# Kernel tuning notes

Measured on AMD Instinct MI355X. Metric: run time of the kernel, lower is better.

The kernel has to match this reference:

```python
import jax, jax.numpy as jnp
import numpy as np
from jax import lax

D_MODEL = 1024
D_STATE = 16
D_CONV = 4
D_INNER = 2 * D_MODEL
BATCH = 2
SEQ = 1024


def setup_inputs() -> dict:
    key = jax.random.key(0)
    ks = jax.random.split(key, 8)
    std = 0.02
    return {
        "x": jax.random.normal(ks[0], (BATCH, SEQ, D_MODEL), jnp.float32),
        "in_proj_w": jax.random.normal(ks[1], (2 * D_INNER, D_MODEL), jnp.float32) * std,
        "conv_w": jax.random.normal(ks[2], (D_INNER, 1, D_CONV), jnp.float32) * 0.1,
        "x_proj_w": jax.random.normal(ks[3], (D_STATE + 1, D_INNER), jnp.float32) * std,
        "dt_w": jax.random.normal(ks[4], (D_INNER, 1), jnp.float32) * std,
        "dt_b": jnp.zeros((D_INNER,), jnp.float32),
        "A_param": jax.random.normal(ks[5], (D_INNER, D_STATE), jnp.float32) * std,
        "D_param": jnp.ones((D_INNER,), jnp.float32),
        "out_w": jax.random.normal(ks[6], (D_MODEL, D_INNER), jnp.float32) * std,
        "out_b": jnp.zeros((D_MODEL,), jnp.float32),
    }


def _silu(v):
    return v * jax.nn.sigmoid(v)


def _mamba_forward(x, in_proj_w, conv_w, x_proj_w, dt_w, dt_b, A_param, D_param, out_w, out_b):
    B, L, _ = x.shape
    # in_proj: [B,L,2*d_inner]
    xz = jnp.einsum('bld,ed->ble', x, in_proj_w)
    u, z = jnp.split(xz, 2, axis=-1)  # each [B,L,d_inner]
    # depthwise causal conv1d along time
    uc = u.transpose(0, 2, 1)  # [B,d_inner,L]
    uc = lax.conv_general_dilated(
        uc, conv_w, window_strides=(1,), padding=[(D_CONV - 1, D_CONV - 1)],
        dimension_numbers=('NCH', 'OIH', 'NCH'), feature_group_count=D_INNER,
    )[:, :, :L]
    u = _silu(uc.transpose(0, 2, 1))  # [B,L,d_inner]
    # x_proj -> (dt scalar, B coeffs)
    x_dbl = jnp.einsum('bld,ed->ble', u, x_proj_w)  # [B,L,d_state+1]
    dt_in = x_dbl[..., :1]                          # [B,L,1]
    Bmat = x_dbl[..., 1:]                           # [B,L,d_state]
    delta = jax.nn.softplus(dt_in * dt_w[:, 0] + dt_b)  # [B,L,d_inner]
    A = -jnp.exp(A_param)                            # [d_inner,d_state]

    # selective scan (time-major lax.scan)
    def step(h, inp):
        d_t, b_t = inp  # [B,d_inner], [B,d_state]
        h = jnp.exp(A * d_t[..., None]) * h + d_t[..., None] * b_t[:, None, :]
        y = jnp.einsum('bdn,bn->bd', h, b_t)
        return h, y

    h0 = jnp.zeros((B, D_INNER, D_STATE), x.dtype)
    _, ys = lax.scan(step, h0, (delta.transpose(1, 0, 2), Bmat.transpose(1, 0, 2)))
    y = ys.transpose(1, 0, 2) + u * D_param  # [B,L,d_inner]
    y = y * _silu(z)
    return jnp.einsum('bld,ed->ble', y, out_w) + out_b


def reference(x, in_proj_w, conv_w, x_proj_w, dt_w, dt_b, A_param, D_param, out_w, out_b):
    return _mamba_forward(x, in_proj_w, conv_w, x_proj_w, dt_w, dt_b, A_param, D_param, out_w, out_b)
```

## Files before the change

kernel.cpp:

```cpp
#include <hip/hip_runtime.h>
#include <stdint.h>
#include <stddef.h>

#define D_MODEL 1024
#define D_STATE 16
#define D_INNER 2048
#define BATCH   2
#define SEQ     1024
#define MROWS   (BATCH*SEQ)

#define NCH 16
#define TCH (SEQ/NCH)
#define NREC (BATCH*D_INNER*D_STATE)

typedef __bf16 bf16x8 __attribute__((ext_vector_type(8)));
typedef float  f32x4  __attribute__((ext_vector_type(4)));
typedef unsigned short u16x8 __attribute__((ext_vector_type(8)));

__device__ __forceinline__ unsigned short f2bf(float f) {
    unsigned int u = __float_as_uint(f);
    u += 0x7fffu + ((u >> 16) & 1u);
    return (unsigned short)(u >> 16);
}
__device__ __forceinline__ float bf2f(unsigned short v) {
    return __uint_as_float((unsigned int)v << 16);
}

__device__ __forceinline__ void gl_lds16(const unsigned short* g, unsigned short* l) {
    __builtin_amdgcn_global_load_lds(
        (const __attribute__((address_space(1))) unsigned int*)g,
        (__attribute__((address_space(3))) unsigned int*)l, 16, 0, 0);
}

__global__ void cvt_all_kernel(const float* __restrict__ x,
                               const float* __restrict__ w1,
                               const float* __restrict__ w2,
                               const float* __restrict__ xw,
                               unsigned short* __restrict__ xb,
                               unsigned short* __restrict__ wbi,
                               unsigned short* __restrict__ wbo,
                               unsigned short* __restrict__ wbp) {
    int blk = blockIdx.x, tid = threadIdx.x;
    if (blk < 8192) {
        const float* src; unsigned short* dst; int i;
        if (blk < 2048)      { src = x;  dst = xb;  i = blk * 1024 + tid * 4; }
        else if (blk < 6144) { src = w1; dst = wbi; i = (blk - 2048) * 1024 + tid * 4; }
        else                 { src = w2; dst = wbo; i = (blk - 6144) * 1024 + tid * 4; }
        float4 v = *(const float4*)(src + i);
        ushort4 o;
        o.x = f2bf(v.x); o.y = f2bf(v.y); o.z = f2bf(v.z); o.w = f2bf(v.w);
        *(ushort4*)(dst + i) = o;
    } else {
        int id = (blk - 8192) * 256 + tid;
        wbp[id] = (id < 17 * D_INNER) ? f2bf(xw[id]) : (unsigned short)0;
    }
}

template<int NT, bool SPLITK2, bool OUT_BF16>
__global__ void gemm_bf16_kernel(const unsigned short* __restrict__ A,
                                 const unsigned short* __restrict__ Bw,
                                 void* __restrict__ Cv,
                                 int M, int N, int K) {
    constexpr int NTW = NT / 32;
    constexpr int BCH = NT / 8;
    __shared__ __align__(16) unsigned short Al[2][2 * 128 * 32];
    __shared__ __align__(16) unsigned short Bl[2][2 * NT * 32];

    const int tid  = threadIdx.x;
    const int lane = tid & 63;
    const int wid  = tid >> 6;
    const int wm   = wid >> 1;
    const int wn   = wid & 1;
    const int ln   = lane & 15;
    const int q    = lane >> 4;
    const int mblk = blockIdx.y * 128;
    const int nblk = blockIdx.x * NT;
    const int srow = lane >> 2;
    const int spart = lane & 3;

    const int kbeg = SPLITK2 ? blockIdx.z * (K / 2) : 0;
    const int kend = SPLITK2 ? kbeg + K / 2 : K;

    f32x4 acc[4][NTW] = {};

    auto stage = [&](int buf, int k0) {
        #pragma unroll
        for (int h = 0; h < 4; ++h) {
            int j = wid * 4 + h;
            int kh = j & 1, rb = j >> 1;
            int row = rb * 16 + srow;
            gl_lds16(A + (size_t)(mblk + row) * K + k0 + kh * 32 + spart * 8,
                     Al[buf] + kh * 4096 + rb * 512);
        }
        #pragma unroll
        for (int h = 0; h < BCH / 4; ++h) {
            int j = wid * (BCH / 4) + h;
            int kh = j & 1, rb = j >> 1;
            int row = rb * 16 + srow;
            gl_lds16(Bw + (size_t)(nblk + row) * K + k0 + kh * 32 + spart * 8,
                     Bl[buf] + kh * (NT * 32) + rb * 512);
        }
    };

    stage(0, kbeg);
    __syncthreads();
    int cur = 0;

    for (int k0 = kbeg; k0 < kend; k0 += 64) {
        if (k0 + 64 < kend) stage(cur ^ 1, k0 + 64);

        #pragma unroll
        for (int kh = 0; kh < 2; ++kh) {
            bf16x8 af[4], bfr[NTW];
            #pragma unroll
            for (int mt = 0; mt < 4; ++mt)
                af[mt] = *(const bf16x8*)(Al[cur] + kh * 4096 + (wm * 64 + mt * 16 + ln) * 32 + q * 8);
            #pragma unroll
            for (int nt = 0; nt < NTW; ++nt)
                bfr[nt] = *(const bf16x8*)(Bl[cur] + kh * (NT * 32) + (wn * (NT/2) + nt * 16 + ln) * 32 + q * 8);
            #pragma unroll
            for (int mt = 0; mt < 4; ++mt)
                #pragma unroll
                for (int nt = 0; nt < NTW; ++nt)
                    acc[mt][nt] = __builtin_amdgcn_mfma_f32_16x16x32_bf16(
                        af[mt], bfr[nt], acc[mt][nt], 0, 0, 0);
        }
        __syncthreads();
        cur ^= 1;
    }

    size_t cofs = SPLITK2 ? (size_t)blockIdx.z * M * N : 0;
    #pragma unroll
    for (int mt = 0; mt < 4; ++mt) {
        #pragma unroll
        for (int nt = 0; nt < NTW; ++nt) {
            int col = nblk + wn * (NT/2) + nt * 16 + ln;
            #pragma unroll
            for (int r = 0; r < 4; ++r) {
                int row = mblk + wm * 64 + mt * 16 + q * 4 + r;
                if (OUT_BF16)
                    ((unsigned short*)Cv)[cofs + (size_t)row * N + col] = f2bf(acc[mt][nt][r]);
                else
                    ((float*)Cv)[cofs + (size_t)row * N + col] = acc[mt][nt][r];
            }
        }
    }
}

__global__ void splitk_reduce_kernel(const float* __restrict__ part,
                                     const float* __restrict__ bias,
                                     float* __restrict__ out) {
    int i = (blockIdx.x * 256 + threadIdx.x) * 4;
    int n = i & (D_MODEL - 1);
    float4 a = *(const float4*)(part + i);
    float4 b = *(const float4*)(part + (size_t)MROWS * D_MODEL + i);
    float4 bv = *(const float4*)(bias + n);
    float4 o;
    o.x = a.x + b.x + bv.x; o.y = a.y + b.y + bv.y;
    o.z = a.z + b.z + bv.z; o.w = a.w + b.w + bv.w;
    *(float4*)(out + i) = o;
}

__global__ void conv_xproj_kernel(const unsigned short* __restrict__ xzb,
                                  const float* __restrict__ conv_w,
                                  const unsigned short* __restrict__ wbp,
                                  unsigned short* __restrict__ ub,
                                  float* __restrict__ dti,
                                  float* __restrict__ Bm) {
    __shared__ float red[4][17];
    const int tid = threadIdx.x;
    const int m = blockIdx.x;
    const int l = m & (SEQ - 1);
    const int d = tid * 8;
    const int lane = tid & 63;
    const int wid  = tid >> 6;

    const float4* wv = (const float4*)(conv_w + (size_t)d * 4);
    float4 w[8];
    #pragma unroll
    for (int e = 0; e < 8; ++e) w[e] = wv[e];
    float s[8] = {0.f, 0.f, 0.f, 0.f, 0.f, 0.f, 0.f, 0.f};
    #pragma unroll
    for (int j = 0; j < 4; ++j) {
        if (l - j >= 0) {
            u16x8 r = *(const u16x8*)(xzb + (size_t)(m - j) * 4096 + d);
            #pragma unroll
            for (int e = 0; e < 8; ++e) {
                float wt = (j == 0) ? w[e].w : (j == 1) ? w[e].z
                         : (j == 2) ? w[e].y : w[e].x;
                s[e] += wt * bf2f(r[e]);
            }
        }
    }
    float u[8];
    u16x8 o;
    #pragma unroll
    for (int e = 0; e < 8; ++e) {
        float sig = 1.f / (1.f + __expf(-s[e]));
        u[e] = s[e] * sig;
        o[e] = f2bf(u[e]);
    }
    *(u16x8*)(ub + (size_t)m * D_INNER + d) = o;

    #pragma unroll
    for (int n = 0; n < 17; ++n) {
        u16x8 wn = *(const u16x8*)(wbp + (size_t)n * D_INNER + d);
        float p = 0.f;
        #pragma unroll
        for (int e = 0; e < 8; ++e) p += u[e] * bf2f(wn[e]);
        #pragma unroll
        for (int off = 32; off > 0; off >>= 1)
            p += __shfl_xor(p, off, 64);
        if (lane == 0) red[wid][n] = p;
    }
    __syncthreads();
    if (tid < 17) {
        float ssum = red[0][tid] + red[1][tid] + red[2][tid] + red[3][tid];
        if (tid == 0) dti[m] = ssum;
        else Bm[(size_t)m * D_STATE + (tid - 1)] = ssum;
    }
}

__device__ __forceinline__ float softplus_f(float xv) {
    return fmaxf(xv, 0.f) + __logf(1.f + __expf(-fabsf(xv)));
}

__global__ void scanA_kernel(const float* __restrict__ dt_in,
                             const float* __restrict__ Bm,
                             const float* __restrict__ dt_w,
                             const float* __restrict__ dt_b,
                             const float* __restrict__ A_param,
                             float* __restrict__ Pg,
                             float* __restrict__ Sg) {
    __shared__ float sdt[TCH];
    __shared__ float sB[TCH * D_STATE];
    const int tid = threadIdx.x;
    const int b = blockIdx.z, c = blockIdx.y;
    const int d = blockIdx.x * 256 + tid;

    if (tid < TCH) sdt[tid] = dt_in[b * SEQ + c * TCH + tid];
    ((float4*)sB)[tid] = ((const float4*)(Bm + ((size_t)(b * SEQ + c * TCH)) * D_STATE))[tid];
    __syncthreads();

    const float dtw = dt_w[d], dtb = dt_b[d];
    float aA[D_STATE], h[D_STATE];
    #pragma unroll
    for (int n4 = 0; n4 < 4; ++n4) {
        float4 ap = ((const float4*)(A_param + (size_t)d * D_STATE))[n4];
        aA[n4*4+0] = -__expf(ap.x); aA[n4*4+1] = -__expf(ap.y);
        aA[n4*4+2] = -__expf(ap.z); aA[n4*4+3] = -__expf(ap.w);
    }
    #pragma unroll
    for (int n = 0; n < D_STATE; ++n) h[n] = 0.f;
    float tsum = 0.f;

    for (int t = 0; t < TCH; ++t) {
        float sp = softplus_f(sdt[t] * dtw + dtb);
        tsum += sp;
        #pragma unroll
        for (int n = 0; n < D_STATE; ++n) {
            float a = __expf(aA[n] * sp);
            h[n] = a * h[n] + sp * sB[t * D_STATE + n];
        }
    }

    size_t base = (size_t)c * NREC + ((size_t)(b * D_INNER + d)) * D_STATE;
    #pragma unroll
    for (int n4 = 0; n4 < 4; ++n4) {
        float4 pv, sv;
        pv.x = __expf(aA[n4*4+0] * tsum); pv.y = __expf(aA[n4*4+1] * tsum);
        pv.z = __expf(aA[n4*4+2] * tsum); pv.w = __expf(aA[n4*4+3] * tsum);
        sv.x = h[n4*4+0]; sv.y = h[n4*4+1]; sv.z = h[n4*4+2]; sv.w = h[n4*4+3];
        *(float4*)(Pg + base + n4 * 4) = pv;
        *(float4*)(Sg + base + n4 * 4) = sv;
    }
}

__global__ void scanB_kernel(const float* __restrict__ Pg,
                             const float* __restrict__ Sg,
                             float* __restrict__ Hin) {
    int idx = blockIdx.x * 256 + threadIdx.x;
    float h = 0.f;
    #pragma unroll
    for (int c = 0; c < NCH; ++c) {
        size_t o = (size_t)c * NREC + idx;
        Hin[o] = h;
        h = Pg[o] * h + Sg[o];
    }
}

__global__ void scanC_kernel(const float* __restrict__ dt_in,
                             const float* __restrict__ Bm,
                             const float* __restrict__ dt_w,
                             const float* __restrict__ dt_b,
                             const float* __restrict__ A_param,
                             const float* __restrict__ Hin,
                             const unsigned short* __restrict__ ub,
                             const unsigned short* __restrict__ xzb,
                             const float* __restrict__ Dp,
                             unsigned short* __restrict__ ypb) {
    __shared__ float sdt[TCH];
    __shared__ float sB[TCH * D_STATE];
    const int tid = threadIdx.x;
    const int b = blockIdx.z, c = blockIdx.y;
    const int d = blockIdx.x * 256 + tid;

    if (tid < TCH) sdt[tid] = dt_in[b * SEQ + c * TCH + tid];
    ((float4*)sB)[tid] = ((const float4*)(Bm + ((size_t)(b * SEQ + c * TCH)) * D_STATE))[tid];
    __syncthreads();

    const float dtw = dt_w[d], dtb = dt_b[d];
    const float Dv = Dp[d];
    float aA[D_STATE], h[D_STATE];
    #pragma unroll
    for (int n4 = 0; n4 < 4; ++n4) {
        float4 ap = ((const float4*)(A_param + (size_t)d * D_STATE))[n4];
        aA[n4*4+0] = -__expf(ap.x); aA[n4*4+1] = -__expf(ap.y);
        aA[n4*4+2] = -__expf(ap.z); aA[n4*4+3] = -__expf(ap.w);
    }
    size_t hbase = (size_t)c * NREC + ((size_t)(b * D_INNER + d)) * D_STATE;
    float h4[D_STATE];
    #pragma unroll
    for (int n4 = 0; n4 < 4; ++n4) {
        float4 hv = *(const float4*)(Hin + hbase + n4 * 4);
        h[n4*4+0] = hv.x; h[n4*4+1] = hv.y; h[n4*4+2] = hv.z; h[n4*4+3] = hv.w;
    }
    (void)h4;

    const size_t mrow0 = (size_t)b * SEQ + c * TCH;
    for (int t = 0; t < TCH; ++t) {
        float sp = softplus_f(sdt[t] * dtw + dtb);
        float y0 = 0.f, y1 = 0.f, y2 = 0.f, y3 = 0.f;
        #pragma unroll
        for (int n4 = 0; n4 < 4; ++n4) {
            #pragma unroll
            for (int j = 0; j < 4; ++j) {
                int n = n4 * 4 + j;
                float Bv = sB[t * D_STATE + n];
                float a = __expf(aA[n] * sp);
                h[n] = a * h[n] + sp * Bv;
                float p = h[n] * Bv;
                if (n4 == 0) y0 += p; else if (n4 == 1) y1 += p;
                else if (n4 == 2) y2 += p; else y3 += p;
            }
        }
        float y = (y0 + y1) + (y2 + y3);
        size_t m = mrow0 + t;
        float z  = bf2f(xzb[m * 4096 + D_INNER + d]);
        float sz = z / (1.f + __expf(-z));
        float uv = bf2f(ub[m * D_INNER + d]);
        ypb[m * D_INNER + d] = f2bf((y + uv * Dv) * sz);
    }
}

extern "C" void kernel_launch(void* const* d_in, const int* in_sizes, int n_in,
                              void* d_out, int out_size, void* d_ws, size_t ws_size,
                              hipStream_t stream) {
    const float* x         = (const float*)d_in[0];
    const float* in_proj_w = (const float*)d_in[1];
    const float* conv_w    = (const float*)d_in[2];
    const float* x_proj_w  = (const float*)d_in[3];
    const float* dt_w      = (const float*)d_in[4];
    const float* dt_b      = (const float*)d_in[5];
    const float* A_param   = (const float*)d_in[6];
    const float* D_param   = (const float*)d_in[7];
    const float* out_w     = (const float*)d_in[8];
    const float* out_b     = (const float*)d_in[9];
    float* out = (float*)d_out;

    char* ws = (char*)d_ws;
    unsigned short* xb  = (unsigned short*)(ws);
    unsigned short* wbi = (unsigned short*)(ws + (4u  << 20));
    unsigned short* wbo = (unsigned short*)(ws + (12u << 20));
    unsigned short* xzb = (unsigned short*)(ws + (16u << 20));
    unsigned short* ub  = (unsigned short*)(ws + (32u << 20));
    float*          dti = (float*)(ws + (40u << 20));
    float*          Bm  = (float*)(ws + (40u << 20) + (64u  << 10));
    unsigned short* wbp = (unsigned short*)(ws + (40u << 20) + (192u << 10));
    float*          Pg  = (float*)(ws + (44u << 20));
    float*          Sg  = (float*)(ws + (52u << 20));
    float*          Hin = (float*)(ws + (60u << 20));
    unsigned short* ypb = (unsigned short*)(ws + (68u << 20));
    float*          g2p = (float*)(ws + (76u << 20));

    cvt_all_kernel<<<dim3(8448), 256, 0, stream>>>(
        x, in_proj_w, out_w, x_proj_w, xb, wbi, wbo, wbp);

    gemm_bf16_kernel<128, false, true><<<dim3(4096 / 128, MROWS / 128), 256, 0, stream>>>(
        xb, wbi, xzb, MROWS, 2 * D_INNER, D_MODEL);

    conv_xproj_kernel<<<dim3(MROWS), 256, 0, stream>>>(xzb, conv_w, wbp, ub, dti, Bm);

    scanA_kernel<<<dim3(D_INNER / 256, NCH, BATCH), 256, 0, stream>>>(
        dti, Bm, dt_w, dt_b, A_param, Pg, Sg);
    scanB_kernel<<<dim3(NREC / 256), 256, 0, stream>>>(Pg, Sg, Hin);
    scanC_kernel<<<dim3(D_INNER / 256, NCH, BATCH), 256, 0, stream>>>(
        dti, Bm, dt_w, dt_b, A_param, Hin, ub, xzb, D_param, ypb);

    gemm_bf16_kernel<64, true, false><<<dim3(1024 / 64, MROWS / 128, 2), 256, 0, stream>>>(
        ypb, wbo, g2p, MROWS, D_MODEL, D_INNER);

    splitk_reduce_kernel<<<dim3(MROWS * D_MODEL / 1024), 256, 0, stream>>>(g2p, out_b, out);
}
```

Baseline: 234.3 us.

## Split scan state across thread pairs and double the time chunks

The chunked selective scan now uses 32 time chunks instead of 16. Each channel's 16 state entries are split across two adjacent threads, so a block covers 128 channels and the grid is four times larger. Each thread's sequential chain shrinks from 64 steps over 16 states to 32 steps over 8 states, which should give the GPU more blocks and shorter dependent chains to hide latency. In exchange, scanC needs a shuffle to combine the two halves, half the lanes sit idle during the output write, and the chunk-combine pass now walks twice as many chunks through a larger carry buffer.

After: 225.8 us. 3.6% less time.

```diff
diff --git a/kernel.cpp b/kernel.cpp
--- a/kernel.cpp
+++ b/kernel.cpp
@@ -9,9 +9,10 @@
 #define SEQ     1024
 #define MROWS   (BATCH*SEQ)
 
-#define NCH 16
+#define NCH 32
 #define TCH (SEQ/NCH)
 #define NREC (BATCH*D_INNER*D_STATE)
+#define DPB 128
 
 typedef __bf16 bf16x8 __attribute__((ext_vector_type(8)));
 typedef float  f32x4  __attribute__((ext_vector_type(4)));
@@ -236,37 +237,40 @@
     __shared__ float sB[TCH * D_STATE];
     const int tid = threadIdx.x;
     const int b = blockIdx.z, c = blockIdx.y;
-    const int d = blockIdx.x * 256 + tid;
+    const int ch = tid >> 1, half = tid & 1;
+    const int d = blockIdx.x * DPB + ch;
 
     if (tid < TCH) sdt[tid] = dt_in[b * SEQ + c * TCH + tid];
-    ((float4*)sB)[tid] = ((const float4*)(Bm + ((size_t)(b * SEQ + c * TCH)) * D_STATE))[tid];
+    if (tid < TCH * D_STATE / 4)
+        ((float4*)sB)[tid] = ((const float4*)(Bm + ((size_t)(b * SEQ + c * TCH)) * D_STATE))[tid];
     __syncthreads();
 
     const float dtw = dt_w[d], dtb = dt_b[d];
-    float aA[D_STATE], h[D_STATE];
-    #pragma unroll
-    for (int n4 = 0; n4 < 4; ++n4) {
-        float4 ap = ((const float4*)(A_param + (size_t)d * D_STATE))[n4];
+    float aA[8], h[8];
+    #pragma unroll
+    for (int n4 = 0; n4 < 2; ++n4) {
+        float4 ap = ((const float4*)(A_param + (size_t)d * D_STATE + half * 8))[n4];
         aA[n4*4+0] = -__expf(ap.x); aA[n4*4+1] = -__expf(ap.y);
         aA[n4*4+2] = -__expf(ap.z); aA[n4*4+3] = -__expf(ap.w);
     }
     #pragma unroll
-    for (int n = 0; n < D_STATE; ++n) h[n] = 0.f;
+    for (int n = 0; n < 8; ++n) h[n] = 0.f;
     float tsum = 0.f;
 
     for (int t = 0; t < TCH; ++t) {
         float sp = softplus_f(sdt[t] * dtw + dtb);
         tsum += sp;
-        #pragma unroll
-        for (int n = 0; n < D_STATE; ++n) {
+        const float* Bt = sB + t * D_STATE + half * 8;
+        #pragma unroll
+        for (int n = 0; n < 8; ++n) {
             float a = __expf(aA[n] * sp);
-            h[n] = a * h[n] + sp * sB[t * D_STATE + n];
-        }
-    }
-
-    size_t base = (size_t)c * NREC + ((size_t)(b * D_INNER + d)) * D_STATE;
-    #pragma unroll
-    for (int n4 = 0; n4 < 4; ++n4) {
+            h[n] = a * h[n] + sp * Bt[n];
+        }
+    }
+
+    size_t base = (size_t)c * NREC + ((size_t)(b * D_INNER + d)) * D_STATE + half * 8;
+    #pragma unroll
+    for (int n4 = 0; n4 < 2; ++n4) {
         float4 pv, sv;
         pv.x = __expf(aA[n4*4+0] * tsum); pv.y = __expf(aA[n4*4+1] * tsum);
         pv.z = __expf(aA[n4*4+2] * tsum); pv.w = __expf(aA[n4*4+3] * tsum);
@@ -303,53 +307,56 @@
     __shared__ float sB[TCH * D_STATE];
     const int tid = threadIdx.x;
     const int b = blockIdx.z, c = blockIdx.y;
-    const int d = blockIdx.x * 256 + tid;
+    const int ch = tid >> 1, half = tid & 1;
+    const int d = blockIdx.x * DPB + ch;
 
     if (tid < TCH) sdt[tid] = dt_in[b * SEQ + c * TCH + tid];
-    ((float4*)sB)[tid] = ((const float4*)(Bm + ((size_t)(b * SEQ + c * TCH)) * D_STATE))[tid];
+    if (tid < TCH * D_STATE / 4)
+        ((float4*)sB)[tid] = ((const float4*)(Bm + ((size_t)(b * SEQ + c * TCH)) * D_STATE))[tid];
     __syncthreads();
 
     const float dtw = dt_w[d], dtb = dt_b[d];
     const float Dv = Dp[d];
-    float aA[D_STATE], h[D_STATE];
-    #pragma unroll
-    for (int n4 = 0; n4 < 4; ++n4) {
-        float4 ap = ((const float4*)(A_param + (size_t)d * D_STATE))[n4];
+    float aA[8], h[8];
+    #pragma unroll
+    for (int n4 = 0; n4 < 2; ++n4) {
+        float4 ap = ((const float4*)(A_param + (size_t)d * D_STATE + half * 8))[n4];
         aA[n4*4+0] = -__expf(ap.x); aA[n4*4+1] = -__expf(ap.y);
         aA[n4*4+2] = -__expf(ap.z); aA[n4*4+3] = -__expf(ap.w);
     }
-    size_t hbase = (size_t)c * NREC + ((size_t)(b * D_INNER + d)) * D_STATE;
-    float h4[D_STATE];
-    #pragma unroll
-    for (int n4 = 0; n4 < 4; ++n4) {
+    size_t hbase = (size_t)c * NREC + ((size_t)(b * D_INNER + d)) * D_STATE + half * 8;
+    #pragma unroll
+    for (int n4 = 0; n4 < 2; ++n4) {
         float4 hv = *(const float4*)(Hin + hbase + n4 * 4);
         h[n4*4+0] = hv.x; h[n4*4+1] = hv.y; h[n4*4+2] = hv.z; h[n4*4+3] = hv.w;
     }
-    (void)h4;
 
     const size_t mrow0 = (size_t)b * SEQ + c * TCH;
     for (int t = 0; t < TCH; ++t) {
         float sp = softplus_f(sdt[t] * dtw + dtb);
-        float y0 = 0.f, y1 = 0.f, y2 = 0.f, y3 = 0.f;
-        #pragma unroll
-        for (int n4 = 0; n4 < 4; ++n4) {
+        const float* Bt = sB + t * D_STATE + half * 8;
+        float y0 = 0.f, y1 = 0.f;
+        #pragma unroll
+        for (int n4 = 0; n4 < 2; ++n4) {
             #pragma unroll
             for (int j = 0; j < 4; ++j) {
                 int n = n4 * 4 + j;
-                float Bv = sB[t * D_STATE + n];
+                float Bv = Bt[n];
                 float a = __expf(aA[n] * sp);
                 h[n] = a * h[n] + sp * Bv;
                 float p = h[n] * Bv;
-                if (n4 == 0) y0 += p; else if (n4 == 1) y1 += p;
-                else if (n4 == 2) y2 += p; else y3 += p;
+                if (n4 == 0) y0 += p; else y1 += p;
             }
         }
-        float y = (y0 + y1) + (y2 + y3);
-        size_t m = mrow0 + t;
-        float z  = bf2f(xzb[m * 4096 + D_INNER + d]);
-        float sz = z / (1.f + __expf(-z));
-        float uv = bf2f(ub[m * D_INNER + d]);
-        ypb[m * D_INNER + d] = f2bf((y + uv * Dv) * sz);
+        float y = y0 + y1;
+        y += __shfl_xor(y, 1, 64);
+        if (half == 0) {
+            size_t m = mrow0 + t;
+            float z  = bf2f(xzb[m * 4096 + D_INNER + d]);
+            float sz = z / (1.f + __expf(-z));
+            float uv = bf2f(ub[m * D_INNER + d]);
+            ypb[m * D_INNER + d] = f2bf((y + uv * Dv) * sz);
+        }
     }
 }
 
@@ -391,10 +398,10 @@
 
     conv_xproj_kernel<<<dim3(MROWS), 256, 0, stream>>>(xzb, conv_w, wbp, ub, dti, Bm);
 
-    scanA_kernel<<<dim3(D_INNER / 256, NCH, BATCH), 256, 0, stream>>>(
+    scanA_kernel<<<dim3(D_INNER / DPB, NCH, BATCH), 256, 0, stream>>>(
         dti, Bm, dt_w, dt_b, A_param, Pg, Sg);
     scanB_kernel<<<dim3(NREC / 256), 256, 0, stream>>>(Pg, Sg, Hin);
-    scanC_kernel<<<dim3(D_INNER / 256, NCH, BATCH), 256, 0, stream>>>(
+    scanC_kernel<<<dim3(D_INNER / DPB, NCH, BATCH), 256, 0, stream>>>(
         dti, Bm, dt_w, dt_b, A_param, Hin, ub, xzb, D_param, ypb);
 
     gemm_bf16_kernel<64, true, false><<<dim3(1024 / 64, MROWS / 128, 2), 256, 0, stream>>>(
```
